# Performance work log

Measured on AMD Instinct MI355X. Metric: run time of the kernel, lower is better.

Reference implementation:

```python
import jax, jax.numpy as jnp
import numpy as np

N_POWER_ITER = 5


def _spectral_normalize(w, n_iter=N_POWER_ITER):
    # w: [out, in] 1x1-conv weight; divide by top singular value (power iteration,
    # deterministic init), mirroring torch.nn.utils.spectral_norm's reparameterization.
    u = jnp.full((w.shape[0],), 1.0 / np.sqrt(w.shape[0]), dtype=w.dtype)
    for _ in range(n_iter):
        v = w.T @ u
        v = v / (jnp.linalg.norm(v) + 1e-12)
        u = w @ v
        u = u / (jnp.linalg.norm(u) + 1e-12)
    sigma = u @ (w @ v)
    return w / sigma


def _maxpool2x2(x):
    # x: [B, C, H, W] -> [B, C, H//2, W//2]
    B, C, H, W = x.shape
    return x.reshape(B, C, H // 2, 2, W // 2, 2).max(axis=(3, 5))


def _conv1x1(w, x):
    # 1x1 conv == channel-mixing einsum. w: [out, in], x: [B, in, H, W]
    return jnp.einsum('oc,bchw->bohw', w, x)


def setup_inputs() -> dict:
    key = jax.random.key(0)
    kx, kq, kk, kv, ko = jax.random.split(key, 5)
    C = 512
    B, H, W = 16, 64, 64
    scale = 0.05
    return {
        'x': jax.random.normal(kx, (B, C, H, W), dtype=jnp.float32),
        'Wq': jax.random.normal(kq, (C // 8, C), dtype=jnp.float32) * scale,
        'Wk': jax.random.normal(kk, (C // 8, C), dtype=jnp.float32) * scale,
        'Wv': jax.random.normal(kv, (C // 2, C), dtype=jnp.float32) * scale,
        'Wo': jax.random.normal(ko, (C, C // 2), dtype=jnp.float32) * scale,
        'gamma': jnp.array([0.5], dtype=jnp.float32),
    }


def reference(x, Wq, Wk, Wv, Wo, gamma):
    B, C, H, W = x.shape
    n_ftrs = H * W
    wq = _spectral_normalize(Wq)
    wk = _spectral_normalize(Wk)
    wv = _spectral_normalize(Wv)
    wo = _spectral_normalize(Wo)
    f = _conv1x1(wq, x).reshape(B, C // 8, n_ftrs)                      # [B, C/8, HW]
    g = _maxpool2x2(_conv1x1(wk, x)).reshape(B, C // 8, n_ftrs // 4)    # [B, C/8, HW/4]
    h = _maxpool2x2(_conv1x1(wv, x)).reshape(B, C // 2, n_ftrs // 4)    # [B, C/2, HW/4]
    # scores: [B, HW, HW/4]; softmax over kv positions
    beta = jax.nn.softmax(jnp.einsum('bcn,bcm->bnm', f, g), axis=-1)
    # attention output: [B, C/2, HW]
    o = jnp.einsum('bcm,bnm->bcn', h, beta).reshape(B, C // 2, H, W)
    o = _conv1x1(wo, o)                                                 # [B, C, H, W]
    return gamma.reshape(()) * o + x
```

## Files before the change

kernel.cpp:

```cpp
#include <hip/hip_runtime.h>
#include <hip/hip_bf16.h>
#include <cstdint>

typedef __attribute__((ext_vector_type(8))) short bf16x8;
typedef __attribute__((ext_vector_type(4))) float f32x4;
typedef __attribute__((ext_vector_type(2))) unsigned int u32x2;

#define B_   16
#define C_   512
#define HW_  4096
#define M3_  384
#define HWP_ 1024
#define CV_  256

__device__ __forceinline__ unsigned short f2b(float f) {
  union { float f; unsigned u; } v; v.f = f;
  unsigned r = v.u + 0x7fffu + ((v.u >> 16) & 1u);
  return (unsigned short)(r >> 16);
}
__device__ __forceinline__ float b2f(unsigned short b) {
  union { unsigned u; float f; } v; v.u = ((unsigned)b) << 16;
  return v.f;
}
__device__ __forceinline__ unsigned pkbf16(float a, float b) {
  __hip_bfloat162 h = __float22bfloat162_rn(make_float2(a, b));
  union { __hip_bfloat162 h; unsigned u; } cv; cv.h = h; return cv.u;
}
__device__ __forceinline__ f32x4 mfma16(bf16x8 a, bf16x8 b, f32x4 c) {
  return __builtin_amdgcn_mfma_f32_16x16x32_bf16(a, b, c, 0, 0, 0);
}
__device__ __forceinline__ void gload_lds16(const unsigned short* g, unsigned short* l) {
  __builtin_amdgcn_global_load_lds(
      (const __attribute__((address_space(1))) void*)g,
      (__attribute__((address_space(3))) void*)l, 16, 0, 0);
}

__global__ __launch_bounds__(256) void k_transpose(const float* __restrict__ x,
                                                   unsigned short* __restrict__ xb) {
  __shared__ unsigned short t[64][66];
  const int b = blockIdx.z, k0 = blockIdx.y * 64, n0 = blockIdx.x * 64;
  const float* xp = x + (size_t)b * C_ * HW_;
  const int ln = threadIdx.x & 63, g = threadIdx.x >> 6;
  for (int kk = g; kk < 64; kk += 4)
    t[kk][ln] = f2b(xp[(size_t)(k0 + kk) * HW_ + n0 + ln]);
  __syncthreads();
  unsigned short* xo = xb + (size_t)b * HW_ * C_;
  for (int nn = g; nn < 64; nn += 4)
    xo[(size_t)(n0 + nn) * C_ + k0 + ln] = t[ln][nn];
}

__global__ __launch_bounds__(256) void k_wtrans(
    const float* __restrict__ Wq, const float* __restrict__ Wk,
    const float* __restrict__ Wv, const float* __restrict__ Wo,
    float* __restrict__ wt) {
  const float* w; int out, in; float* dst;
  switch (blockIdx.z) {
    case 0: w = Wq; out = 64;  in = 512; dst = wt;          break;
    case 1: w = Wk; out = 64;  in = 512; dst = wt + 32768;  break;
    case 2: w = Wv; out = 256; in = 512; dst = wt + 65536;  break;
    default: w = Wo; out = 512; in = 256; dst = wt + 196608; break;
  }
  const int o0 = blockIdx.y * 64, i0 = blockIdx.x * 64;
  if (o0 >= out || i0 >= in) return;
  __shared__ float t[64][65];
  const int ln = threadIdx.x & 63, g = threadIdx.x >> 6;
  for (int oo = g; oo < 64; oo += 4)
    t[oo][ln] = w[(size_t)(o0 + oo) * in + i0 + ln];
  __syncthreads();
  for (int ii = g; ii < 64; ii += 4)
    dst[(size_t)(i0 + ii) * out + o0 + ln] = t[ln][ii];
}

__device__ __forceinline__ float breduce1024(float val, float* red) {
  __syncthreads();
#pragma unroll
  for (int off = 32; off > 0; off >>= 1) val += __shfl_down(val, off);
  if ((threadIdx.x & 63) == 0) red[threadIdx.x >> 6] = val;
  __syncthreads();
  float s = 0.f;
#pragma unroll
  for (int i = 0; i < 16; ++i) s += red[i];
  return s;
}

__global__ __launch_bounds__(1024) void k_specnorm(
    const float* __restrict__ Wq, const float* __restrict__ Wk,
    const float* __restrict__ Wv, const float* __restrict__ Wo,
    const float* __restrict__ wt,
    unsigned short* __restrict__ wqkv, unsigned short* __restrict__ wob) {
  __shared__ float u[512], v[512];
  __shared__ float part[4096];
  __shared__ float red[16];
  const float* w; const float* wT; int out, in; unsigned short* dst;
  switch (blockIdx.x) {
    case 0: w = Wq; wT = wt;          out = 64;  in = 512; dst = wqkv;             break;
    case 1: w = Wk; wT = wt + 32768;  out = 64;  in = 512; dst = wqkv + 64 * 512;  break;
    case 2: w = Wv; wT = wt + 65536;  out = 256; in = 512; dst = wqkv + 128 * 512; break;
    default: w = Wo; wT = wt + 196608; out = 512; in = 256; dst = wob;             break;
  }
  const int tid = threadIdx.x;
  const float rs = rsqrtf((float)out);
  if (tid < out) u[tid] = rs;
  __syncthreads();
  for (int it = 0; it < 5; ++it) {
    {
      const int G = in >> 2, nch = 1024 / G;
      const int ch = tid / G, grp = tid - ch * G;
      const int rpc = out / nch, obase = ch * rpc;
      f32x4 acc = {0.f, 0.f, 0.f, 0.f};
#pragma unroll 8
      for (int r = 0; r < rpc; ++r) {
        const int o = obase + r;
        const f32x4 wv = *reinterpret_cast<const f32x4*>(&w[(size_t)o * in + grp * 4]);
        const float uo = u[o];
        acc[0] += wv[0] * uo; acc[1] += wv[1] * uo;
        acc[2] += wv[2] * uo; acc[3] += wv[3] * uo;
      }
      *reinterpret_cast<f32x4*>(&part[ch * in + grp * 4]) = acc;
      __syncthreads();
      if (tid < in) {
        float s = 0.f;
        for (int c2 = 0; c2 < nch; ++c2) s += part[c2 * in + tid];
        v[tid] = s;
      }
    }
    {
      float ss = 0.f;
      __syncthreads();
      if (tid < in) ss = v[tid] * v[tid];
      ss = breduce1024(ss, red);
      const float sv = 1.f / (sqrtf(ss) + 1e-12f);
      if (tid < in) v[tid] *= sv;
      __syncthreads();
    }
    {
      const int G = out >> 2, nch = 1024 / G;
      const int ch = tid / G, grp = tid - ch * G;
      const int cpc = in / nch, cbase = ch * cpc;
      f32x4 acc = {0.f, 0.f, 0.f, 0.f};
#pragma unroll 8
      for (int r = 0; r < cpc; ++r) {
        const int c = cbase + r;
        const f32x4 wv = *reinterpret_cast<const f32x4*>(&wT[(size_t)c * out + grp * 4]);
        const float vc = v[c];
        acc[0] += wv[0] * vc; acc[1] += wv[1] * vc;
        acc[2] += wv[2] * vc; acc[3] += wv[3] * vc;
      }
      *reinterpret_cast<f32x4*>(&part[ch * out + grp * 4]) = acc;
      __syncthreads();
      if (tid < out) {
        float s = 0.f;
        for (int c2 = 0; c2 < nch; ++c2) s += part[c2 * out + tid];
        u[tid] = s;
      }
    }
    {
      float su = 0.f;
      __syncthreads();
      if (tid < out) su = u[tid] * u[tid];
      su = breduce1024(su, red);
      const float sv2 = 1.f / (sqrtf(su) + 1e-12f);
      if (tid < out) u[tid] *= sv2;
      __syncthreads();
    }
  }
  float sp = 0.f;
  {
    const int G = out >> 2, nch = 1024 / G;
    const int ch = tid / G, grp = tid - ch * G;
    const int cpc = in / nch, cbase = ch * cpc;
    f32x4 acc = {0.f, 0.f, 0.f, 0.f};
#pragma unroll 8
    for (int r = 0; r < cpc; ++r) {
      const int c = cbase + r;
      const f32x4 wv = *reinterpret_cast<const f32x4*>(&wT[(size_t)c * out + grp * 4]);
      const float vc = v[c];
      acc[0] += wv[0] * vc; acc[1] += wv[1] * vc;
      acc[2] += wv[2] * vc; acc[3] += wv[3] * vc;
    }
    *reinterpret_cast<f32x4*>(&part[ch * out + grp * 4]) = acc;
    __syncthreads();
    if (tid < out) {
      float s = 0.f;
      for (int c2 = 0; c2 < nch; ++c2) s += part[c2 * out + tid];
      sp = s * u[tid];
    }
  }
  sp = breduce1024(sp, red);
  const float oscale = (blockIdx.x == 0) ? 1.44269504f : 1.0f;
  const float inv_sigma = (1.f / sp) * oscale;
  const int total = out * in;
  for (int i = tid * 4; i < total; i += 4096) {
    const f32x4 wv = *reinterpret_cast<const f32x4*>(&w[i]);
    u32x2 pw;
    pw[0] = ((unsigned)f2b(wv[1] * inv_sigma) << 16) | f2b(wv[0] * inv_sigma);
    pw[1] = ((unsigned)f2b(wv[3] * inv_sigma) << 16) | f2b(wv[2] * inv_sigma);
    *reinterpret_cast<u32x2*>(&dst[i]) = pw;
  }
}

__global__ __launch_bounds__(256) void k_gemm_qkv(
    const unsigned short* __restrict__ xb, const unsigned short* __restrict__ wqkv,
    unsigned short* __restrict__ yt) {
  __shared__ alignas(16) char smem[32768];
  unsigned short* As = (unsigned short*)smem;
  unsigned short* Bs = (unsigned short*)(smem + 16384);
  const int lid = blockIdx.x;
  const int swz = (lid & 7) * 192 + (lid >> 3);
  const int mt = swz % 3, rest = swz / 3;
  const int nt = rest & 31, b = rest >> 5;
  const int n0 = nt * 128, m0 = mt * 128;
  const unsigned short* Ap = xb + (size_t)b * HW_ * C_ + (size_t)n0 * C_;
  const unsigned short* Bp = wqkv + (size_t)m0 * C_;
  const int tid = threadIdx.x, lane = tid & 63, wid = tid >> 6;
  const int wn = (wid >> 1) * 64, wm = (wid & 1) * 64;
  f32x4 acc[4][4] = {};
  for (int k0 = 0; k0 < C_; k0 += 64) {
    __syncthreads();
#pragma unroll
    for (int i = 0; i < 4; ++i) {
      const int r = i * 32 + (tid >> 3);
      const int s = tid & 7;
      const int rw = i * 32 + wid * 8;
      const size_t goff = (size_t)r * C_ + k0 + (size_t)((s ^ (r & 7)) * 8);
      gload_lds16(&Ap[goff], &As[rw * 64]);
      gload_lds16(&Bp[goff], &Bs[rw * 64]);
    }
    __syncthreads();
#pragma unroll
    for (int kk = 0; kk < 2; ++kk) {
      bf16x8 af[4], bfr[4];
#pragma unroll
      for (int i = 0; i < 4; ++i) {
        const int r = wn + i * 16 + (lane & 15);
        const int slot = (kk * 4 + (lane >> 4)) ^ (r & 7);
        af[i] = *reinterpret_cast<const bf16x8*>(&As[r * 64 + slot * 8]);
      }
#pragma unroll
      for (int j = 0; j < 4; ++j) {
        const int r = wm + j * 16 + (lane & 15);
        const int slot = (kk * 4 + (lane >> 4)) ^ (r & 7);
        bfr[j] = *reinterpret_cast<const bf16x8*>(&Bs[r * 64 + slot * 8]);
      }
#pragma unroll
      for (int i = 0; i < 4; ++i)
#pragma unroll
        for (int j = 0; j < 4; ++j) acc[i][j] = mfma16(af[i], bfr[j], acc[i][j]);
    }
  }
  unsigned short* eps = (unsigned short*)smem;
  unsigned short* Y = yt + (size_t)b * HW_ * M3_;
#pragma unroll
  for (int h = 0; h < 2; ++h) {
    __syncthreads();
    if ((wid >> 1) == h) {
#pragma unroll
      for (int i = 0; i < 4; ++i)
#pragma unroll
        for (int j = 0; j < 4; ++j)
#pragma unroll
          for (int r = 0; r < 4; ++r) {
            const int nl = i * 16 + (lane >> 4) * 4 + r;
            const int ml = wm + j * 16 + (lane & 15);
            eps[nl * 136 + ml] = f2b(acc[i][j][r]);
          }
    }
    __syncthreads();
#pragma unroll
    for (int t = 0; t < 4; ++t) {
      const int row = t * 16 + (tid >> 4);
      const int m8 = (tid & 15) * 8;
      *reinterpret_cast<f32x4*>(&Y[(size_t)(n0 + h * 64 + row) * M3_ + m0 + m8]) =
          *reinterpret_cast<const f32x4*>(&eps[row * 136 + m8]);
    }
  }
}

__global__ __launch_bounds__(256) void k_pool_g(const unsigned short* __restrict__ yt,
                                                unsigned short* __restrict__ gt) {
  const int b = blockIdx.y, mp0 = blockIdx.x * 64;
  const int c = threadIdx.x & 63, dm = threadIdx.x >> 6;
  const unsigned short* Y = yt + (size_t)b * HW_ * M3_;
  unsigned short* G = gt + (size_t)b * HWP_ * 64;
  for (int mm = dm; mm < 64; mm += 4) {
    const int mp = mp0 + mm;
    const int n00 = (mp >> 5) * 128 + (mp & 31) * 2;
    const float a0 = b2f(Y[(size_t)n00 * M3_ + 64 + c]);
    const float a1 = b2f(Y[(size_t)(n00 + 1) * M3_ + 64 + c]);
    const float a2 = b2f(Y[(size_t)(n00 + 64) * M3_ + 64 + c]);
    const float a3 = b2f(Y[(size_t)(n00 + 65) * M3_ + 64 + c]);
    G[(size_t)mp * 64 + c] = f2b(fmaxf(fmaxf(a0, a1), fmaxf(a2, a3)));
  }
}

__global__ __launch_bounds__(256) void k_pool_vt(const unsigned short* __restrict__ yt,
                                                 unsigned short* __restrict__ vt) {
  __shared__ unsigned short t[64][66];
  const int b = blockIdx.z, mp0 = blockIdx.x * 64, cv0 = blockIdx.y * 64;
  const unsigned short* Y = yt + (size_t)b * HW_ * M3_;
  const int c = threadIdx.x & 63, dm = threadIdx.x >> 6;
  for (int mm = dm; mm < 64; mm += 4) {
    const int mp = mp0 + mm;
    const int n00 = (mp >> 5) * 128 + (mp & 31) * 2;
    const float a0 = b2f(Y[(size_t)n00 * M3_ + 128 + cv0 + c]);
    const float a1 = b2f(Y[(size_t)(n00 + 1) * M3_ + 128 + cv0 + c]);
    const float a2 = b2f(Y[(size_t)(n00 + 64) * M3_ + 128 + cv0 + c]);
    const float a3 = b2f(Y[(size_t)(n00 + 65) * M3_ + 128 + cv0 + c]);
    t[mm][c] = f2b(fmaxf(fmaxf(a0, a1), fmaxf(a2, a3)));
  }
  __syncthreads();
  unsigned short* V = vt + (size_t)b * CV_ * HWP_;
  for (int cc = dm; cc < 64; cc += 4)
    V[(size_t)(cv0 + cc) * HWP_ + mp0 + c] = t[c][cc];
}

__global__ __launch_bounds__(512, 4) void k_attn(
    const unsigned short* __restrict__ yt, const unsigned short* __restrict__ gt,
    const unsigned short* __restrict__ vt, unsigned short* __restrict__ oat) {
  __shared__ alignas(16) char smem[59392];
  const int lid = blockIdx.x;
  const int swz = (lid & 7) * 64 + (lid >> 3);
  const int q0 = (swz & 31) * 128, b = swz >> 5;
  const int tid = threadIdx.x, lane = tid & 63, wid = tid >> 6;
  const int q = lane & 15, g = lane >> 4;
  const unsigned short* Qg = yt + (size_t)b * HW_ * M3_ + (size_t)(q0 + wid * 16) * M3_;
  const unsigned short* Gg = gt + (size_t)b * HWP_ * 64;
  const unsigned short* Vg = vt + (size_t)b * CV_ * HWP_;
  unsigned short* P = (unsigned short*)(smem + 49152) + wid * 640;
  bf16x8 qf[2];
#pragma unroll
  for (int kk = 0; kk < 2; ++kk)
    qf[kk] = *reinterpret_cast<const bf16x8*>(&Qg[(size_t)q * M3_ + kk * 32 + g * 8]);
  const int kr = tid >> 3, ks = tid & 7;
  f32x4 kreg, vreg[2];
  if (tid < 256) kreg = *reinterpret_cast<const f32x4*>(&Gg[(size_t)kr * 64 + ks * 8]);
  const unsigned short* vp0;
  const unsigned short* vp1;
  {
    const int i0c = tid, r0 = i0c >> 2, s0 = i0c & 3;
    const int i1c = tid + 512, r1 = i1c >> 2, s1 = i1c & 3;
    vp0 = Vg + (size_t)r0 * HWP_ + s0 * 8;
    vp1 = Vg + (size_t)r1 * HWP_ + s1 * 8;
    vreg[0] = *reinterpret_cast<const f32x4*>(vp0);
    vreg[1] = *reinterpret_cast<const f32x4*>(vp1);
  }
  {
    unsigned short* Kb = (unsigned short*)smem;
    unsigned short* Vb = (unsigned short*)(smem + 8192);
    if (tid < 256)
      *reinterpret_cast<f32x4*>(&Kb[kr * 64 + (ks ^ (kr & 7)) * 8]) = kreg;
    const int i0c = tid, r0 = i0c >> 2, s0 = i0c & 3;
    const int i1c = tid + 512, r1 = i1c >> 2, s1 = i1c & 3;
    *reinterpret_cast<f32x4*>(&Vb[r0 * 40 + s0 * 8]) = vreg[0];
    *reinterpret_cast<f32x4*>(&Vb[r1 * 40 + s1 * 8]) = vreg[1];
  }
  const unsigned short* kp = Gg + (size_t)(32 + kr) * 64 + ks * 8;
  if (tid < 256) kreg = *reinterpret_cast<const f32x4*>(kp);
  kp += 2048;
  vp0 += 32; vp1 += 32;
  vreg[0] = *reinterpret_cast<const f32x4*>(vp0);
  vreg[1] = *reinterpret_cast<const f32x4*>(vp1);
  vp0 += 32; vp1 += 32;
  __syncthreads();
  f32x4 oacc[16] = {};
  float m_run = -1e30f, l_part = 0.f;
#pragma unroll 2
  for (int it = 0; it < 32; ++it) {
    const int cur = it & 1;
    unsigned short* Kc = (unsigned short*)(smem + cur * 4096);
    unsigned short* Vc = (unsigned short*)(smem + 8192 + cur * 20480);
    if (it < 31) {
      unsigned short* Kn = (unsigned short*)(smem + (cur ^ 1) * 4096);
      unsigned short* Vn = (unsigned short*)(smem + 8192 + (cur ^ 1) * 20480);
      if (tid < 256)
        *reinterpret_cast<f32x4*>(&Kn[kr * 64 + (ks ^ (kr & 7)) * 8]) = kreg;
      const int i0c = tid, r0 = i0c >> 2, s0 = i0c & 3;
      const int i1c = tid + 512, r1 = i1c >> 2, s1 = i1c & 3;
      *reinterpret_cast<f32x4*>(&Vn[r0 * 40 + s0 * 8]) = vreg[0];
      *reinterpret_cast<f32x4*>(&Vn[r1 * 40 + s1 * 8]) = vreg[1];
    }
    if (it < 30) {
      if (tid < 256) kreg = *reinterpret_cast<const f32x4*>(kp);
      kp += 2048;
      vreg[0] = *reinterpret_cast<const f32x4*>(vp0);
      vreg[1] = *reinterpret_cast<const f32x4*>(vp1);
      vp0 += 32; vp1 += 32;
    }
    f32x4 sacc[2] = {};
#pragma unroll
    for (int kk = 0; kk < 2; ++kk) {
      bf16x8 kf[2];
#pragma unroll
      for (int i = 0; i < 2; ++i) {
        const int row = i * 16 + q;
        const int sl = (kk * 4 + g) ^ (row & 7);
        kf[i] = *reinterpret_cast<const bf16x8*>(&Kc[row * 64 + sl * 8]);
      }
#pragma unroll
      for (int i = 0; i < 2; ++i) sacc[i] = mfma16(kf[i], qf[kk], sacc[i]);
    }
    float tmax = fmaxf(fmaxf(fmaxf(sacc[0][0], sacc[0][1]), fmaxf(sacc[0][2], sacc[0][3])),
                       fmaxf(fmaxf(sacc[1][0], sacc[1][1]), fmaxf(sacc[1][2], sacc[1][3])));
    tmax = fmaxf(tmax, __shfl_xor(tmax, 16));
    tmax = fmaxf(tmax, __shfl_xor(tmax, 32));
    if (__any(tmax > m_run + 11.0f)) {
      const float mnew = fmaxf(m_run, tmax);
      const float alpha = exp2f(m_run - mnew);
      m_run = mnew;
      l_part *= alpha;
      float al[4];
#pragma unroll
      for (int r = 0; r < 4; ++r) al[r] = __shfl(alpha, g * 4 + r);
#pragma unroll
      for (int j = 0; j < 16; ++j) {
        oacc[j][0] *= al[0]; oacc[j][1] *= al[1];
        oacc[j][2] *= al[2]; oacc[j][3] *= al[3];
      }
    }
#pragma unroll
    for (int i = 0; i < 2; ++i) {
      const float p0 = exp2f(sacc[i][0] - m_run);
      const float p1 = exp2f(sacc[i][1] - m_run);
      const float p2 = exp2f(sacc[i][2] - m_run);
      const float p3 = exp2f(sacc[i][3] - m_run);
      l_part += (p0 + p1) + (p2 + p3);
      u32x2 pw;
      pw[0] = pkbf16(p0, p1);
      pw[1] = pkbf16(p2, p3);
      *reinterpret_cast<u32x2*>(&P[q * 40 + i * 16 + g * 4]) = pw;
    }
    __builtin_amdgcn_s_setprio(1);
    const bf16x8 pa = *reinterpret_cast<const bf16x8*>(&P[q * 40 + g * 8]);
#pragma unroll
    for (int j = 0; j < 16; ++j) {
      const int row = j * 16 + q;
      const bf16x8 vf = *reinterpret_cast<const bf16x8*>(&Vc[row * 40 + g * 8]);
      oacc[j] = mfma16(pa, vf, oacc[j]);
    }
    __builtin_amdgcn_s_setprio(0);
    __syncthreads();
  }
  float lsum = l_part;
  lsum += __shfl_xor(lsum, 16);
  lsum += __shfl_xor(lsum, 32);
  float linv[4];
  {
    const float myinv = 1.f / lsum;
#pragma unroll
    for (int r = 0; r < 4; ++r) linv[r] = __shfl(myinv, g * 4 + r);
  }
  unsigned short* eps = (unsigned short*)smem;
  unsigned short* O = oat + (size_t)b * HW_ * CV_ + (size_t)q0 * CV_;
#pragma unroll
  for (int ch = 0; ch < 2; ++ch) {
    __syncthreads();
    if ((wid >> 2) == ch) {
#pragma unroll
      for (int j = 0; j < 16; ++j)
#pragma unroll
        for (int r = 0; r < 4; ++r) {
          const int row = (wid & 3) * 16 + g * 4 + r;
          const int cv = j * 16 + q;
          eps[row * 264 + cv] = f2b(oacc[j][r] * linv[r]);
        }
    }
    __syncthreads();
#pragma unroll
    for (int t = 0; t < 4; ++t) {
      const int row = t * 16 + (tid >> 5);
      const int cv8 = (tid & 31) * 8;
      *reinterpret_cast<f32x4*>(&O[(size_t)(ch * 64 + row) * CV_ + cv8]) =
          *reinterpret_cast<const f32x4*>(&eps[row * 264 + cv8]);
    }
  }
}

__global__ __launch_bounds__(256) void k_gemm_out(
    const unsigned short* __restrict__ oat, const unsigned short* __restrict__ wob,
    const float* __restrict__ x, const float* __restrict__ gamma,
    float* __restrict__ out) {
  __shared__ alignas(16) char smem[32768];
  unsigned short* As = (unsigned short*)smem;
  unsigned short* Bs = (unsigned short*)(smem + 16384);
  const int lid = blockIdx.x;
  const int swz = (lid & 7) * 256 + (lid >> 3);
  const int ct = swz & 3, nt = (swz >> 2) & 31, b = swz >> 7;
  const int n0 = nt * 128, co0 = ct * 128;
  const unsigned short* Ap = wob + (size_t)co0 * CV_;
  const unsigned short* Bp = oat + (size_t)b * HW_ * CV_ + (size_t)n0 * CV_;
  const int tid = threadIdx.x, lane = tid & 63, wid = tid >> 6;
  const int wc = (wid >> 1) * 64, wn = (wid & 1) * 64;
  f32x4 acc[4][4] = {};
  for (int k0 = 0; k0 < CV_; k0 += 64) {
    __syncthreads();
#pragma unroll
    for (int i = 0; i < 4; ++i) {
      const int r = i * 32 + (tid >> 3);
      const int s = tid & 7;
      const int rw = i * 32 + wid * 8;
      const size_t goff = (size_t)r * CV_ + k0 + (size_t)((s ^ (r & 7)) * 8);
      gload_lds16(&Ap[goff], &As[rw * 64]);
      gload_lds16(&Bp[goff], &Bs[rw * 64]);
    }
    __syncthreads();
#pragma unroll
    for (int kk = 0; kk < 2; ++kk) {
      bf16x8 af[4], bfr[4];
#pragma unroll
      for (int i = 0; i < 4; ++i) {
        const int r = wc + i * 16 + (lane & 15);
        const int slot = (kk * 4 + (lane >> 4)) ^ (r & 7);
        af[i] = *reinterpret_cast<const bf16x8*>(&As[r * 64 + slot * 8]);
      }
#pragma unroll
      for (int j = 0; j < 4; ++j) {
        const int r = wn + j * 16 + (lane & 15);
        const int slot = (kk * 4 + (lane >> 4)) ^ (r & 7);
        bfr[j] = *reinterpret_cast<const bf16x8*>(&Bs[r * 64 + slot * 8]);
      }
#pragma unroll
      for (int i = 0; i < 4; ++i)
#pragma unroll
        for (int j = 0; j < 4; ++j) acc[i][j] = mfma16(af[i], bfr[j], acc[i][j]);
    }
  }
  float* eps = (float*)smem;
  const float g = gamma[0];
  const size_t base = (size_t)b * C_ * HW_;
#pragma unroll
  for (int h = 0; h < 4; ++h) {
    __syncthreads();
    if ((wid >> 1) == (h >> 1)) {
#pragma unroll
      for (int ii = 0; ii < 2; ++ii) {
        const int i = (h & 1) * 2 + ii;
#pragma unroll
        for (int j = 0; j < 4; ++j)
#pragma unroll
          for (int r = 0; r < 4; ++r) {
            const int col2 = ii * 16 + (lane >> 4) * 4 + r;
            const int nl = wn + j * 16 + (lane & 15);
            eps[col2 * 132 + nl] = acc[i][j][r];
          }
      }
    }
    __syncthreads();
#pragma unroll
    for (int t = 0; t < 4; ++t) {
      const int row = t * 8 + (tid >> 5);
      const int col = (tid & 31) * 4;
      const size_t goff = base + (size_t)(co0 + h * 32 + row) * HW_ + n0 + col;
      const f32x4 xv = *reinterpret_cast<const f32x4*>(&x[goff]);
      const f32x4 av = *reinterpret_cast<const f32x4*>(&eps[row * 132 + col]);
      f32x4 ov;
      ov[0] = g * av[0] + xv[0];
      ov[1] = g * av[1] + xv[1];
      ov[2] = g * av[2] + xv[2];
      ov[3] = g * av[3] + xv[3];
      *reinterpret_cast<f32x4*>(&out[goff]) = ov;
    }
  }
}

extern "C" void kernel_launch(void* const* d_in, const int* in_sizes, int n_in,
                              void* d_out, int out_size, void* d_ws, size_t ws_size,
                              hipStream_t stream) {
  (void)in_sizes; (void)n_in; (void)out_size; (void)ws_size;
  const float* x     = (const float*)d_in[0];
  const float* Wq    = (const float*)d_in[1];
  const float* Wk    = (const float*)d_in[2];
  const float* Wv    = (const float*)d_in[3];
  const float* Wo    = (const float*)d_in[4];
  const float* gamma = (const float*)d_in[5];
  float* out = (float*)d_out;
  char* ws = (char*)d_ws;

  unsigned short* wqkv = (unsigned short*)(ws);
  unsigned short* wob  = (unsigned short*)(ws + 393216);
  unsigned short* xb   = (unsigned short*)(ws + 655360);
  unsigned short* yt   = (unsigned short*)(ws + 67764224);
  unsigned short* gt   = (unsigned short*)(ws + 118095872);
  unsigned short* vt   = (unsigned short*)(ws + 120193024);
  unsigned short* oat  = xb;
  float* wt = (float*)yt;

  k_transpose<<<dim3(64, 8, 16), 256, 0, stream>>>(x, xb);
  k_wtrans<<<dim3(8, 8, 4), 256, 0, stream>>>(Wq, Wk, Wv, Wo, wt);
  k_specnorm<<<4, 1024, 0, stream>>>(Wq, Wk, Wv, Wo, wt, wqkv, wob);
  k_gemm_qkv<<<1536, 256, 0, stream>>>(xb, wqkv, yt);
  k_pool_g<<<dim3(16, 16), 256, 0, stream>>>(yt, gt);
  k_pool_vt<<<dim3(16, 4, 16), 256, 0, stream>>>(yt, vt);
  k_attn<<<512, 512, 0, stream>>>(yt, gt, vt, oat);
  k_gemm_out<<<2048, 256, 0, stream>>>(oat, wob, x, gamma, out);
}
```

Baseline: 298.1 us.

## Fuse 2x2 maxpool of K and V into the QKV GEMM epilogue

The QKV projection GEMM epilogue now performs the 2x2 max-pooling for the key and value channels directly from its shared-memory staging tile. It writes pooled G and transposed V straight to global memory, and stores only the query columns in a narrower 64-wide buffer. This drops the two separate pooling kernels and the write-then-reread of the full 384-channel intermediate. The cost is a more complex epilogue with extra syncs and shared-memory traffic, and the design depends on each 128-row tile covering exactly two image rows.

New measurement: 281.3 us. 5.7% less time.

```diff
diff --git a/kernel.cpp b/kernel.cpp
--- a/kernel.cpp
+++ b/kernel.cpp
@@ -5,6 +5,7 @@
 typedef __attribute__((ext_vector_type(8))) short bf16x8;
 typedef __attribute__((ext_vector_type(4))) float f32x4;
 typedef __attribute__((ext_vector_type(2))) unsigned int u32x2;
+typedef __attribute__((ext_vector_type(4))) unsigned int u32x4;
 
 #define B_   16
 #define C_   512
@@ -201,7 +202,8 @@
 
 __global__ __launch_bounds__(256) void k_gemm_qkv(
     const unsigned short* __restrict__ xb, const unsigned short* __restrict__ wqkv,
-    unsigned short* __restrict__ yt) {
+    unsigned short* __restrict__ ytq, unsigned short* __restrict__ gt,
+    unsigned short* __restrict__ vt) {
   __shared__ alignas(16) char smem[32768];
   unsigned short* As = (unsigned short*)smem;
   unsigned short* Bs = (unsigned short*)(smem + 16384);
@@ -249,7 +251,12 @@
     }
   }
   unsigned short* eps = (unsigned short*)smem;
-  unsigned short* Y = yt + (size_t)b * HW_ * M3_;
+  float* pmk = (float*)(smem + 20480);
+  unsigned short* pmv = (unsigned short*)(smem + 20480);
+  const int mp0 = nt * 32;
+  unsigned short* Yq = ytq + (size_t)b * HW_ * 64;
+  unsigned short* Gp = gt + (size_t)b * HWP_ * 64;
+  unsigned short* Vp = vt + (size_t)b * CV_ * HWP_;
 #pragma unroll
   for (int h = 0; h < 2; ++h) {
     __syncthreads();
@@ -266,56 +273,75 @@
           }
     }
     __syncthreads();
-#pragma unroll
-    for (int t = 0; t < 4; ++t) {
-      const int row = t * 16 + (tid >> 4);
-      const int m8 = (tid & 15) * 8;
-      *reinterpret_cast<f32x4*>(&Y[(size_t)(n0 + h * 64 + row) * M3_ + m0 + m8]) =
-          *reinterpret_cast<const f32x4*>(&eps[row * 136 + m8]);
-    }
-  }
-}
-
-__global__ __launch_bounds__(256) void k_pool_g(const unsigned short* __restrict__ yt,
-                                                unsigned short* __restrict__ gt) {
-  const int b = blockIdx.y, mp0 = blockIdx.x * 64;
-  const int c = threadIdx.x & 63, dm = threadIdx.x >> 6;
-  const unsigned short* Y = yt + (size_t)b * HW_ * M3_;
-  unsigned short* G = gt + (size_t)b * HWP_ * 64;
-  for (int mm = dm; mm < 64; mm += 4) {
-    const int mp = mp0 + mm;
-    const int n00 = (mp >> 5) * 128 + (mp & 31) * 2;
-    const float a0 = b2f(Y[(size_t)n00 * M3_ + 64 + c]);
-    const float a1 = b2f(Y[(size_t)(n00 + 1) * M3_ + 64 + c]);
-    const float a2 = b2f(Y[(size_t)(n00 + 64) * M3_ + 64 + c]);
-    const float a3 = b2f(Y[(size_t)(n00 + 65) * M3_ + 64 + c]);
-    G[(size_t)mp * 64 + c] = f2b(fmaxf(fmaxf(a0, a1), fmaxf(a2, a3)));
-  }
-}
-
-__global__ __launch_bounds__(256) void k_pool_vt(const unsigned short* __restrict__ yt,
-                                                 unsigned short* __restrict__ vt) {
-  __shared__ unsigned short t[64][66];
-  const int b = blockIdx.z, mp0 = blockIdx.x * 64, cv0 = blockIdx.y * 64;
-  const unsigned short* Y = yt + (size_t)b * HW_ * M3_;
-  const int c = threadIdx.x & 63, dm = threadIdx.x >> 6;
-  for (int mm = dm; mm < 64; mm += 4) {
-    const int mp = mp0 + mm;
-    const int n00 = (mp >> 5) * 128 + (mp & 31) * 2;
-    const float a0 = b2f(Y[(size_t)n00 * M3_ + 128 + cv0 + c]);
-    const float a1 = b2f(Y[(size_t)(n00 + 1) * M3_ + 128 + cv0 + c]);
-    const float a2 = b2f(Y[(size_t)(n00 + 64) * M3_ + 128 + cv0 + c]);
-    const float a3 = b2f(Y[(size_t)(n00 + 65) * M3_ + 128 + cv0 + c]);
-    t[mm][c] = f2b(fmaxf(fmaxf(a0, a1), fmaxf(a2, a3)));
+    if (mt == 0) {
+      {
+        const int row = tid >> 2, qc = (tid & 3) * 16;
+        *reinterpret_cast<f32x4*>(&Yq[(size_t)(n0 + h * 64 + row) * 64 + qc]) =
+            *reinterpret_cast<const f32x4*>(&eps[row * 136 + qc]);
+        *reinterpret_cast<f32x4*>(&Yq[(size_t)(n0 + h * 64 + row) * 64 + qc + 8]) =
+            *reinterpret_cast<const f32x4*>(&eps[row * 136 + qc + 8]);
+      }
+      {
+        const int j = tid >> 3, mg = tid & 7;
+        const bf16x8 a = *reinterpret_cast<const bf16x8*>(&eps[(2 * j) * 136 + 64 + mg * 8]);
+        const bf16x8 bb = *reinterpret_cast<const bf16x8*>(&eps[(2 * j + 1) * 136 + 64 + mg * 8]);
+        float* pd = &pmk[j * 68 + mg * 8];
+#pragma unroll
+        for (int e = 0; e < 8; ++e) {
+          const float m2 = fmaxf(b2f((unsigned short)a[e]), b2f((unsigned short)bb[e]));
+          pd[e] = (h == 0) ? m2 : fmaxf(pd[e], m2);
+        }
+      }
+    } else {
+#pragma unroll
+      for (int t2 = 0; t2 < 2; ++t2) {
+        const int it = tid + t2 * 256;
+        const int j = it >> 4, mg = it & 15;
+        const bf16x8 a = *reinterpret_cast<const bf16x8*>(&eps[(2 * j) * 136 + mg * 8]);
+        const bf16x8 bb = *reinterpret_cast<const bf16x8*>(&eps[(2 * j + 1) * 136 + mg * 8]);
+        float m8[8];
+#pragma unroll
+        for (int e = 0; e < 8; ++e)
+          m8[e] = fmaxf(b2f((unsigned short)a[e]), b2f((unsigned short)bb[e]));
+        unsigned short* pv = &pmv[j * 136 + mg * 8];
+        if (h == 1) {
+          const bf16x8 prev = *reinterpret_cast<const bf16x8*>(pv);
+#pragma unroll
+          for (int e = 0; e < 8; ++e) m8[e] = fmaxf(m8[e], b2f((unsigned short)prev[e]));
+        }
+        u32x4 w;
+        w[0] = pkbf16(m8[0], m8[1]); w[1] = pkbf16(m8[2], m8[3]);
+        w[2] = pkbf16(m8[4], m8[5]); w[3] = pkbf16(m8[6], m8[7]);
+        *reinterpret_cast<u32x4*>(pv) = w;
+      }
+    }
   }
   __syncthreads();
-  unsigned short* V = vt + (size_t)b * CV_ * HWP_;
-  for (int cc = dm; cc < 64; cc += 4)
-    V[(size_t)(cv0 + cc) * HWP_ + mp0 + c] = t[c][cc];
+  if (mt == 0) {
+    const int j = tid >> 3, ck0 = (tid & 7) * 8;
+    const float* ps = &pmk[j * 68 + ck0];
+    u32x4 w;
+    w[0] = pkbf16(ps[0], ps[1]); w[1] = pkbf16(ps[2], ps[3]);
+    w[2] = pkbf16(ps[4], ps[5]); w[3] = pkbf16(ps[6], ps[7]);
+    *reinterpret_cast<u32x4*>(&Gp[(size_t)(mp0 + j) * 64 + ck0]) = w;
+  } else {
+    const int cv0 = (mt - 1) * 128;
+    const int ml = tid >> 1, j0 = (tid & 1) * 16;
+    unsigned w[8];
+#pragma unroll
+    for (int p = 0; p < 8; ++p) {
+      const unsigned lo = pmv[(j0 + 2 * p) * 136 + ml];
+      const unsigned hi = pmv[(j0 + 2 * p + 1) * 136 + ml];
+      w[p] = lo | (hi << 16);
+    }
+    unsigned short* dst = &Vp[(size_t)(cv0 + ml) * HWP_ + mp0 + j0];
+    *reinterpret_cast<u32x4*>(dst) = *reinterpret_cast<u32x4*>(&w[0]);
+    *reinterpret_cast<u32x4*>(dst + 8) = *reinterpret_cast<u32x4*>(&w[4]);
+  }
 }
 
 __global__ __launch_bounds__(512, 4) void k_attn(
-    const unsigned short* __restrict__ yt, const unsigned short* __restrict__ gt,
+    const unsigned short* __restrict__ ytq, const unsigned short* __restrict__ gt,
     const unsigned short* __restrict__ vt, unsigned short* __restrict__ oat) {
   __shared__ alignas(16) char smem[59392];
   const int lid = blockIdx.x;
@@ -323,14 +349,14 @@
   const int q0 = (swz & 31) * 128, b = swz >> 5;
   const int tid = threadIdx.x, lane = tid & 63, wid = tid >> 6;
   const int q = lane & 15, g = lane >> 4;
-  const unsigned short* Qg = yt + (size_t)b * HW_ * M3_ + (size_t)(q0 + wid * 16) * M3_;
+  const unsigned short* Qg = ytq + (size_t)b * HW_ * 64 + (size_t)(q0 + wid * 16) * 64;
   const unsigned short* Gg = gt + (size_t)b * HWP_ * 64;
   const unsigned short* Vg = vt + (size_t)b * CV_ * HWP_;
   unsigned short* P = (unsigned short*)(smem + 49152) + wid * 640;
   bf16x8 qf[2];
 #pragma unroll
   for (int kk = 0; kk < 2; ++kk)
-    qf[kk] = *reinterpret_cast<const bf16x8*>(&Qg[(size_t)q * M3_ + kk * 32 + g * 8]);
+    qf[kk] = *reinterpret_cast<const bf16x8*>(&Qg[(size_t)q * 64 + kk * 32 + g * 8]);
   const int kr = tid >> 3, ks = tid & 7;
   f32x4 kreg, vreg[2];
   if (tid < 256) kreg = *reinterpret_cast<const f32x4*>(&Gg[(size_t)kr * 64 + ks * 8]);
@@ -578,18 +604,16 @@
   unsigned short* wqkv = (unsigned short*)(ws);
   unsigned short* wob  = (unsigned short*)(ws + 393216);
   unsigned short* xb   = (unsigned short*)(ws + 655360);
-  unsigned short* yt   = (unsigned short*)(ws + 67764224);
+  unsigned short* ytq  = (unsigned short*)(ws + 67764224);
   unsigned short* gt   = (unsigned short*)(ws + 118095872);
   unsigned short* vt   = (unsigned short*)(ws + 120193024);
   unsigned short* oat  = xb;
-  float* wt = (float*)yt;
+  float* wt = (float*)ytq;
 
   k_transpose<<<dim3(64, 8, 16), 256, 0, stream>>>(x, xb);
   k_wtrans<<<dim3(8, 8, 4), 256, 0, stream>>>(Wq, Wk, Wv, Wo, wt);
   k_specnorm<<<4, 1024, 0, stream>>>(Wq, Wk, Wv, Wo, wt, wqkv, wob);
-  k_gemm_qkv<<<1536, 256, 0, stream>>>(xb, wqkv, yt);
-  k_pool_g<<<dim3(16, 16), 256, 0, stream>>>(yt, gt);
-  k_pool_vt<<<dim3(16, 4, 16), 256, 0, stream>>>(yt, vt);
-  k_attn<<<512, 512, 0, stream>>>(yt, gt, vt, oat);
+  k_gemm_qkv<<<1536, 256, 0, stream>>>(xb, wqkv, ytq, gt, vt);
+  k_attn<<<512, 512, 0, stream>>>(ytq, gt, vt, oat);
   k_gemm_out<<<2048, 256, 0, stream>>>(oat, wob, x, gamma, out);
 }
```
